# Kernel optimization log

Hardware: AMD Instinct MI355X
Metric: run time of the kernel (lower is better)

Reference implementation:

```python
import jax, jax.numpy as jnp
import numpy as np

B, N, C, H = 8, 128, 256, 8
HS = C // H
SCALE = HS ** -0.5
EPS = 1e-5


def layernorm(x, w, b):
    mu = jnp.mean(x, axis=-1, keepdims=True)
    var = jnp.var(x, axis=-1, keepdims=True)
    return (x - mu) * jax.lax.rsqrt(var + EPS) * w + b


def setup_inputs() -> dict:
    key = jax.random.key(0)
    ks = jax.random.split(key, 12)
    inp = {
        "joint_feature": jax.random.normal(ks[0], (B, N, C), jnp.float32),
        "relation_feature": jax.random.normal(ks[1], (B, N, N, C), jnp.float32),
        "conn_feature": jax.random.uniform(ks[2], (B, N, N), jnp.float32),
        # LayerNorm params
        "ln1_w": jnp.ones((C,), jnp.float32), "ln1_b": jnp.zeros((C,), jnp.float32),
        "ln2_w": jnp.ones((C,), jnp.float32), "ln2_b": jnp.zeros((C,), jnp.float32),
        "ln3_w": jnp.ones((C,), jnp.float32), "ln3_b": jnp.zeros((C,), jnp.float32),
        # Attention params (qkv_bias=False)
        "qkv_w": 0.02 * jax.random.normal(ks[3], (3 * C, C), jnp.float32),
        "rconv_w": 0.02 * jax.random.normal(ks[4], (H, C), jnp.float32),
        "proj_w": 0.02 * jax.random.normal(ks[5], (C, C), jnp.float32),
        "proj_b": jnp.zeros((C,), jnp.float32),
        # Mlp params (hidden_features == dim in this Block)
        "fc1_w": 0.02 * jax.random.normal(ks[6], (C, C), jnp.float32),
        "fc1_b": jnp.zeros((C,), jnp.float32),
        "fc2_w": 0.02 * jax.random.normal(ks[7], (C, C), jnp.float32),
        "fc2_b": jnp.zeros((C,), jnp.float32),
    }
    return inp


def reference(joint_feature, relation_feature, conn_feature,
              ln1_w, ln1_b, ln2_w, ln2_b, ln3_w, ln3_b,
              qkv_w, rconv_w, proj_w, proj_b,
              fc1_w, fc1_b, fc2_w, fc2_b):
    # --- Attention branch ---
    jn = layernorm(joint_feature, ln1_w, ln1_b)          # [B,N,C]
    rn = layernorm(relation_feature, ln2_w, ln2_b)       # [B,N,N,C]
    qkv = jn @ qkv_w.T                                   # [B,N,3C]
    qkv = qkv.reshape(B, N, 3, H, HS)
    q = jnp.transpose(qkv[:, :, 0], (0, 2, 1, 3))        # [B,H,N,HS]
    k = jnp.transpose(qkv[:, :, 1], (0, 2, 1, 3))
    v = jnp.transpose(qkv[:, :, 2], (0, 2, 1, 3))
    attn_J = jnp.einsum('bhnd,bhmd->bhnm', q, k)         # [B,H,N,N]
    attn_R = jnp.einsum('bnmc,hc->bhnm', rn, rconv_w)    # [B,H,N,N]
    attn = (attn_J + attn_R) * conn_feature[:, None] * SCALE
    attn = jax.nn.softmax(attn, axis=-1)
    x = jnp.einsum('bhnm,bhmd->bnhd', attn, v).reshape(B, N, C)
    x = x @ proj_w.T + proj_b
    joint = joint_feature + x
    # --- MLP branch (hidden = dim, exact GELU as torch nn.GELU) ---
    h = layernorm(joint, ln3_w, ln3_b)
    h = jax.nn.gelu(h @ fc1_w.T + fc1_b, approximate=False)
    h = h @ fc2_w.T + fc2_b
    return joint + h
```

## Files before the change

kernel.cpp:

```cpp
#include <hip/hip_runtime.h>
#include <hip/hip_bf16.h>

#define Bb 8
#define Nn 128
#define Cc 256
#define SCALE 0.1767766952966369f
#define EPS 1e-5f

typedef short v8s __attribute__((ext_vector_type(8)));
typedef short v4s __attribute__((ext_vector_type(4)));
typedef float v4f __attribute__((ext_vector_type(4)));
using bf16_t = __hip_bfloat16;

__device__ inline float bf2f(bf16_t h){ return __bfloat162float(h); }
__device__ inline short f2bfbits(float f){
    unsigned int u = __float_as_uint(f);
    u += 0x7fff + ((u >> 16) & 1u);
    return (short)(u >> 16);
}

__device__ inline float rscatter8(const float (&S)[8], int l){
    bool b0 = l & 1, b1 = l & 2, b2 = l & 4;
    float t[4];
#pragma unroll
    for (int k = 0; k < 4; k++){
        float keep = b0 ? S[k+4] : S[k];
        float give = b0 ? S[k]   : S[k+4];
        t[k] = keep + __shfl_xor(give, 1);
    }
    float u[2];
#pragma unroll
    for (int k = 0; k < 2; k++){
        float keep = b1 ? t[k+2] : t[k];
        float give = b1 ? t[k]   : t[k+2];
        u[k] = keep + __shfl_xor(give, 2);
    }
    float r;
    {
        float keep = b2 ? u[1] : u[0];
        float give = b2 ? u[0] : u[1];
        r = keep + __shfl_xor(give, 4);
    }
    r += __shfl_xor(r, 8);
    r += __shfl_xor(r, 16);
    return r;
}

template<int NTOT, int EPI>
__device__ __forceinline__ void lngemm_body(
        const float* __restrict__ A, const float* __restrict__ lnw,
        const float* __restrict__ lnb, const float* __restrict__ W,
        const float* __restrict__ bias, short* __restrict__ out,
        int mtile, int ntile0)
{
    __shared__ short a_s[16][264];
    __shared__ float red[2][16][16];
    const int t = threadIdx.x;
    const int r = t >> 4, j = t & 15;
    const float* rowp = A + (size_t)(mtile + r) * Cc + j * 16;
    float x[16];
#pragma unroll
    for (int i = 0; i < 4; i++){
        float4 v = *(const float4*)(rowp + i * 4);
        x[i*4+0]=v.x; x[i*4+1]=v.y; x[i*4+2]=v.z; x[i*4+3]=v.w;
    }
    float s1 = 0.f, s2 = 0.f;
#pragma unroll
    for (int i = 0; i < 16; i++){ s1 += x[i]; s2 = fmaf(x[i], x[i], s2); }
    red[0][r][j] = s1; red[1][r][j] = s2;
    __syncthreads();
    float t1 = 0.f, t2 = 0.f;
#pragma unroll
    for (int i = 0; i < 16; i++){ t1 += red[0][r][i]; t2 += red[1][r][i]; }
    const float mu = t1 * (1.f/256.f);
    const float rstd = rsqrtf(t2 * (1.f/256.f) - mu*mu + EPS);
    short pk[16];
#pragma unroll
    for (int i = 0; i < 4; i++){
        float4 wv4 = *(const float4*)(lnw + j*16 + i*4);
        float4 bv4 = *(const float4*)(lnb + j*16 + i*4);
        pk[i*4+0] = f2bfbits((x[i*4+0]-mu)*rstd*wv4.x + bv4.x);
        pk[i*4+1] = f2bfbits((x[i*4+1]-mu)*rstd*wv4.y + bv4.y);
        pk[i*4+2] = f2bfbits((x[i*4+2]-mu)*rstd*wv4.z + bv4.z);
        pk[i*4+3] = f2bfbits((x[i*4+3]-mu)*rstd*wv4.w + bv4.w);
    }
    *(v8s*)&a_s[r][j*16]     = *(v8s*)&pk[0];
    *(v8s*)&a_s[r][j*16 + 8] = *(v8s*)&pk[8];
    __syncthreads();

    const int lane = t & 63;
    const int wv = t >> 6;
    const int ntile = ntile0 + wv * 16;
    const int mi = lane & 15, q = lane >> 4;
    const short* alds = &a_s[mi][q * 8];
    const float* wp = W + (size_t)(ntile + mi) * Cc + q * 8;
    v4f acc = {0.f, 0.f, 0.f, 0.f};
#pragma unroll
    for (int kk = 0; kk < 8; kk++){
        v8s af = *(const v8s*)(alds + kk * 32);
        float4 w0 = *(const float4*)(wp + kk * 32);
        float4 w1 = *(const float4*)(wp + kk * 32 + 4);
        v8s bf;
        bf[0]=f2bfbits(w0.x); bf[1]=f2bfbits(w0.y); bf[2]=f2bfbits(w0.z); bf[3]=f2bfbits(w0.w);
        bf[4]=f2bfbits(w1.x); bf[5]=f2bfbits(w1.y); bf[6]=f2bfbits(w1.z); bf[7]=f2bfbits(w1.w);
        acc = __builtin_amdgcn_mfma_f32_16x16x32_bf16(af, bf, acc, 0, 0, 0);
    }
    const int n = ntile + mi;
    const float bia = (EPI == 2) ? bias[n] : 0.f;
#pragma unroll
    for (int rr = 0; rr < 4; rr++){
        int m = mtile + q * 4 + rr;
        float v = acc[rr] + bia;
        if (EPI == 2) v = 0.5f * v * (1.f + erff(v * 0.70710678118654752f));
        out[(size_t)m * NTOT + n] = f2bfbits(v);
    }
}

__global__ __launch_bounds__(256) void mega1_kernel(
        const float* __restrict__ rel,
        const float* __restrict__ ln2w, const float* __restrict__ ln2b,
        const float* __restrict__ rconv, short* __restrict__ R,
        const float* __restrict__ joint,
        const float* __restrict__ ln1w, const float* __restrict__ ln1b,
        const float* __restrict__ qkvw, short* __restrict__ qkvb)
{
    if (blockIdx.x >= 2048){
        const int bx = blockIdx.x - 2048;
        lngemm_body<768, 0>(joint, ln1w, ln1b, qkvw, nullptr, qkvb,
                            (bx & 63) * 16, (bx >> 6) * 64);
        return;
    }
    const int lane = threadIdx.x & 63;
    const int hl = lane & 31;
    const int c0 = hl * 8;

    float w2[8][8];
    float Tp[8] = {0,0,0,0,0,0,0,0};
    float Bp[8] = {0,0,0,0,0,0,0,0};
#pragma unroll
    for (int j = 0; j < 8; j++){
        float lw = ln2w[c0 + j];
        float lb = ln2b[c0 + j];
#pragma unroll
        for (int hh = 0; hh < 8; hh++){
            float rc = rconv[hh * Cc + c0 + j];
            w2[j][hh] = lw * rc;
            Tp[hh] += w2[j][hh];
            Bp[hh] = fmaf(lb, rc, Bp[hh]);
        }
    }
    const float Th = rscatter8(Tp, hl);
    const float Bh = rscatter8(Bp, hl);
    const int h = (hl & 1) * 4 + ((hl >> 1) & 1) * 2 + ((hl >> 2) & 1);

    const int hw = (blockIdx.x * 256 + threadIdx.x) >> 5;
    const int hwStride = (2048 * 256) >> 5;
    const int totalRows = Bb * Nn * Nn;

    for (int row = hw; row < totalRows; row += hwStride){
        const float* rp = rel + (size_t)row * Cc + c0;
        float4 xa = *(const float4*)(rp);
        float4 xb = *(const float4*)(rp + 4);
        float x[8] = { xa.x, xa.y, xa.z, xa.w, xb.x, xb.y, xb.z, xb.w };
        float sum = 0.f, sq = 0.f;
        float S[8] = {0,0,0,0,0,0,0,0};
#pragma unroll
        for (int j = 0; j < 8; j++){
            float xv = x[j];
            sum += xv;
            sq = fmaf(xv, xv, sq);
#pragma unroll
            for (int hh = 0; hh < 8; hh++)
                S[hh] = fmaf(xv, w2[j][hh], S[hh]);
        }
#pragma unroll
        for (int o = 1; o <= 16; o <<= 1){
            sum += __shfl_xor(sum, o);
            sq  += __shfl_xor(sq,  o);
        }
        float mu = sum * (1.f / 256.f);
        float rstd = rsqrtf(sq * (1.f / 256.f) - mu * mu + EPS);
        float Sh = rscatter8(S, hl);
        if (hl < 8)
            R[(size_t)row * 8 + h] = f2bfbits(rstd * (Sh - mu * Th) + Bh);
    }
}

template<int EPI>
__global__ __launch_bounds__(256) void gemm_kernel(
        const bf16_t* __restrict__ A, const float* __restrict__ W,
        const float* __restrict__ bias, const float* __restrict__ res,
        float* __restrict__ out)
{
    const int lane = threadIdx.x & 63;
    const int wv = threadIdx.x >> 6;
    const int mtile = blockIdx.x * 16;
    const int ntile = blockIdx.y * 64 + wv * 16;
    const int mi = lane & 15, q = lane >> 4;
    const bf16_t* ap = A + (size_t)(mtile + mi) * Cc + q * 8;
    const float* wp = W + (size_t)(ntile + mi) * Cc + q * 8;
    v4f acc = {0.f, 0.f, 0.f, 0.f};
#pragma unroll
    for (int kk = 0; kk < 8; kk++){
        v8s af = *(const v8s*)(ap + kk * 32);
        float4 w0 = *(const float4*)(wp + kk * 32);
        float4 w1 = *(const float4*)(wp + kk * 32 + 4);
        v8s bf;
        bf[0]=f2bfbits(w0.x); bf[1]=f2bfbits(w0.y); bf[2]=f2bfbits(w0.z); bf[3]=f2bfbits(w0.w);
        bf[4]=f2bfbits(w1.x); bf[5]=f2bfbits(w1.y); bf[6]=f2bfbits(w1.z); bf[7]=f2bfbits(w1.w);
        acc = __builtin_amdgcn_mfma_f32_16x16x32_bf16(af, bf, acc, 0, 0, 0);
    }
    const int n = ntile + mi;
    const float bia = bias[n];
#pragma unroll
    for (int r = 0; r < 4; r++){
        int m = mtile + q * 4 + r;
        float v = acc[r] + bia + res[(size_t)m * Cc + n];
        out[(size_t)m * Cc + n] = v;
    }
}

__global__ __launch_bounds__(256) void fc1_kernel(
        const float* __restrict__ joint2,
        const float* __restrict__ ln3w, const float* __restrict__ ln3b,
        const float* __restrict__ fc1w, const float* __restrict__ fc1b,
        short* __restrict__ h2)
{
    lngemm_body<256, 2>(joint2, ln3w, ln3b, fc1w, fc1b, h2,
                        blockIdx.x * 16, blockIdx.y * 64);
}

__global__ __launch_bounds__(256) void attn_kernel(
        const bf16_t* __restrict__ qkv,
        const bf16_t* __restrict__ R,
        const float* __restrict__ conn,
        short* __restrict__ xatt)
{
    const int bid = blockIdx.x;
    const int b = bid >> 5;
    const int h = (bid >> 2) & 7;
    const int nq = bid & 3;
    __shared__ float k_s[128 * 36];
    __shared__ float v_s[128 * 32];
    __shared__ float q_s[32 * 33];
    __shared__ float p_s[32 * 132];
    const int t = threadIdx.x;
    const bf16_t* qkvb = qkv + (size_t)b * Nn * 768;

#pragma unroll
    for (int i = 0; i < 16; i++){
        int idx = t + i * 256;
        int m = idx >> 5, d = idx & 31;
        k_s[m * 36 + d] = bf2f(qkvb[m * 768 + 256 + h * 32 + d]);
        v_s[m * 32 + d] = bf2f(qkvb[m * 768 + 512 + h * 32 + d]);
    }
#pragma unroll
    for (int i = 0; i < 4; i++){
        int idx = t + i * 256;
        int nl = idx >> 5, d = idx & 31;
        q_s[nl * 33 + d] = bf2f(qkvb[(nq * 32 + nl) * 768 + h * 32 + d]);
    }
    __syncthreads();

    const int nl = t >> 3, tg = t & 7;
    const int n = nq * 32 + nl;
    float qr[32];
#pragma unroll
    for (int d = 0; d < 32; d++) qr[d] = q_s[nl * 33 + d];
    const bf16_t* Rrow = R + ((size_t)(b * Nn + n) * Nn) * 8 + h;
    const float* crow = conn + (size_t)(b * Nn + n) * Nn;

    float s[16];
#pragma unroll
    for (int i = 0; i < 16; i++){
        int m = tg + 8 * i;
        float acc = 0.f;
#pragma unroll
        for (int g = 0; g < 8; g++){
            float4 kv = *(const float4*)&k_s[m * 36 + g * 4];
            acc = fmaf(qr[g*4+0], kv.x, acc);
            acc = fmaf(qr[g*4+1], kv.y, acc);
            acc = fmaf(qr[g*4+2], kv.z, acc);
            acc = fmaf(qr[g*4+3], kv.w, acc);
        }
        s[i] = (acc + bf2f(Rrow[(size_t)m * 8])) * crow[m] * SCALE;
    }
    float mx = s[0];
#pragma unroll
    for (int i = 1; i < 16; i++) mx = fmaxf(mx, s[i]);
    mx = fmaxf(mx, __shfl_xor(mx, 1));
    mx = fmaxf(mx, __shfl_xor(mx, 2));
    mx = fmaxf(mx, __shfl_xor(mx, 4));
    float lsum = 0.f;
#pragma unroll
    for (int i = 0; i < 16; i++){ s[i] = expf(s[i] - mx); lsum += s[i]; }
    lsum += __shfl_xor(lsum, 1);
    lsum += __shfl_xor(lsum, 2);
    lsum += __shfl_xor(lsum, 4);
    float inv = 1.f / lsum;
#pragma unroll
    for (int i = 0; i < 16; i++)
        p_s[nl * 132 + tg + 8 * i] = s[i] * inv;
    __syncthreads();

    const int d0 = tg * 4;
    float a0 = 0.f, a1 = 0.f, a2 = 0.f, a3 = 0.f;
    for (int m = 0; m < 128; m++){
        float p = p_s[nl * 132 + m];
        float4 vv = *(const float4*)&v_s[m * 32 + d0];
        a0 = fmaf(p, vv.x, a0);
        a1 = fmaf(p, vv.y, a1);
        a2 = fmaf(p, vv.z, a2);
        a3 = fmaf(p, vv.w, a3);
    }
    v4s o4; o4[0]=f2bfbits(a0); o4[1]=f2bfbits(a1); o4[2]=f2bfbits(a2); o4[3]=f2bfbits(a3);
    *(v4s*)(xatt + (size_t)(b * Nn + n) * Cc + h * 32 + d0) = o4;
}

extern "C" void kernel_launch(void* const* d_in, const int* in_sizes, int n_in,
                              void* d_out, int out_size, void* d_ws, size_t ws_size,
                              hipStream_t stream)
{
    const float* joint  = (const float*)d_in[0];
    const float* rel    = (const float*)d_in[1];
    const float* conn   = (const float*)d_in[2];
    const float* ln1w   = (const float*)d_in[3];
    const float* ln1b   = (const float*)d_in[4];
    const float* ln2w   = (const float*)d_in[5];
    const float* ln2b   = (const float*)d_in[6];
    const float* ln3w   = (const float*)d_in[7];
    const float* ln3b   = (const float*)d_in[8];
    const float* qkvw   = (const float*)d_in[9];
    const float* rconv  = (const float*)d_in[10];
    const float* projw  = (const float*)d_in[11];
    const float* projb  = (const float*)d_in[12];
    const float* fc1w   = (const float*)d_in[13];
    const float* fc1b   = (const float*)d_in[14];
    const float* fc2w   = (const float*)d_in[15];
    const float* fc2b   = (const float*)d_in[16];

    char* w = (char*)d_ws;
    short* Rb     = (short*)(w);
    short* qkvb   = (short*)(w + 2097152);
    short* xattb  = (short*)(w + 3670016);
    float* joint2 = (float*)(w + 4194304);
    short* h2b    = (short*)(w + 5242880);

    mega1_kernel<<<dim3(2816), dim3(256), 0, stream>>>(
        rel, ln2w, ln2b, rconv, Rb, joint, ln1w, ln1b, qkvw, qkvb);
    attn_kernel<<<dim3(256), dim3(256), 0, stream>>>(
        (const bf16_t*)qkvb, (const bf16_t*)Rb, conn, xattb);
    gemm_kernel<1><<<dim3(64, 4), dim3(256), 0, stream>>>(
        (const bf16_t*)xattb, projw, projb, joint, joint2);
    fc1_kernel<<<dim3(64, 4), dim3(256), 0, stream>>>(
        joint2, ln3w, ln3b, fc1w, fc1b, h2b);
    gemm_kernel<3><<<dim3(64, 4), dim3(256), 0, stream>>>(
        (const bf16_t*)h2b, fc2w, fc2b, joint2, (float*)d_out);
}
```

Before: 258.7 us.

## Fuse proj, LN3, fc1+GELU and fc2 into one tail kernel per row tile

Replaces three separate launches (proj GEMM with residual, LN3+fc1+GELU, fc2 GEMM with residual) with a single tail kernel. Each block owns 16 rows and all 256 output columns, keeping joint2 and the hidden activations in shared memory instead of round-tripping through global workspace. This removes two launches and the intermediate global traffic. In exchange, the grid shrinks from 256 to 64 blocks, which lowers parallelism, and each block now reads the full weight matrices.

```diff
diff --git a/kernel.cpp b/kernel.cpp
--- a/kernel.cpp
+++ b/kernel.cpp
@@ -46,12 +46,11 @@
     return r;
 }
 
-template<int NTOT, int EPI>
+template<int NTOT>
 __device__ __forceinline__ void lngemm_body(
         const float* __restrict__ A, const float* __restrict__ lnw,
         const float* __restrict__ lnb, const float* __restrict__ W,
-        const float* __restrict__ bias, short* __restrict__ out,
-        int mtile, int ntile0)
+        short* __restrict__ out, int mtile, int ntile0)
 {
     __shared__ short a_s[16][264];
     __shared__ float red[2][16][16];
@@ -106,13 +105,10 @@
         acc = __builtin_amdgcn_mfma_f32_16x16x32_bf16(af, bf, acc, 0, 0, 0);
     }
     const int n = ntile + mi;
-    const float bia = (EPI == 2) ? bias[n] : 0.f;
 #pragma unroll
     for (int rr = 0; rr < 4; rr++){
         int m = mtile + q * 4 + rr;
-        float v = acc[rr] + bia;
-        if (EPI == 2) v = 0.5f * v * (1.f + erff(v * 0.70710678118654752f));
-        out[(size_t)m * NTOT + n] = f2bfbits(v);
+        out[(size_t)m * NTOT + n] = f2bfbits(acc[rr]);
     }
 }
 
@@ -126,8 +122,8 @@
 {
     if (blockIdx.x >= 2048){
         const int bx = blockIdx.x - 2048;
-        lngemm_body<768, 0>(joint, ln1w, ln1b, qkvw, nullptr, qkvb,
-                            (bx & 63) * 16, (bx >> 6) * 64);
+        lngemm_body<768>(joint, ln1w, ln1b, qkvw, qkvb,
+                         (bx & 63) * 16, (bx >> 6) * 64);
         return;
     }
     const int lane = threadIdx.x & 63;
@@ -184,50 +180,6 @@
         if (hl < 8)
             R[(size_t)row * 8 + h] = f2bfbits(rstd * (Sh - mu * Th) + Bh);
     }
-}
-
-template<int EPI>
-__global__ __launch_bounds__(256) void gemm_kernel(
-        const bf16_t* __restrict__ A, const float* __restrict__ W,
-        const float* __restrict__ bias, const float* __restrict__ res,
-        float* __restrict__ out)
-{
-    const int lane = threadIdx.x & 63;
-    const int wv = threadIdx.x >> 6;
-    const int mtile = blockIdx.x * 16;
-    const int ntile = blockIdx.y * 64 + wv * 16;
-    const int mi = lane & 15, q = lane >> 4;
-    const bf16_t* ap = A + (size_t)(mtile + mi) * Cc + q * 8;
-    const float* wp = W + (size_t)(ntile + mi) * Cc + q * 8;
-    v4f acc = {0.f, 0.f, 0.f, 0.f};
-#pragma unroll
-    for (int kk = 0; kk < 8; kk++){
-        v8s af = *(const v8s*)(ap + kk * 32);
-        float4 w0 = *(const float4*)(wp + kk * 32);
-        float4 w1 = *(const float4*)(wp + kk * 32 + 4);
-        v8s bf;
-        bf[0]=f2bfbits(w0.x); bf[1]=f2bfbits(w0.y); bf[2]=f2bfbits(w0.z); bf[3]=f2bfbits(w0.w);
-        bf[4]=f2bfbits(w1.x); bf[5]=f2bfbits(w1.y); bf[6]=f2bfbits(w1.z); bf[7]=f2bfbits(w1.w);
-        acc = __builtin_amdgcn_mfma_f32_16x16x32_bf16(af, bf, acc, 0, 0, 0);
-    }
-    const int n = ntile + mi;
-    const float bia = bias[n];
-#pragma unroll
-    for (int r = 0; r < 4; r++){
-        int m = mtile + q * 4 + r;
-        float v = acc[r] + bia + res[(size_t)m * Cc + n];
-        out[(size_t)m * Cc + n] = v;
-    }
-}
-
-__global__ __launch_bounds__(256) void fc1_kernel(
-        const float* __restrict__ joint2,
-        const float* __restrict__ ln3w, const float* __restrict__ ln3b,
-        const float* __restrict__ fc1w, const float* __restrict__ fc1b,
-        short* __restrict__ h2)
-{
-    lngemm_body<256, 2>(joint2, ln3w, ln3b, fc1w, fc1b, h2,
-                        blockIdx.x * 16, blockIdx.y * 64);
 }
 
 __global__ __launch_bounds__(256) void attn_kernel(
@@ -315,6 +267,148 @@
     }
     v4s o4; o4[0]=f2bfbits(a0); o4[1]=f2bfbits(a1); o4[2]=f2bfbits(a2); o4[3]=f2bfbits(a3);
     *(v4s*)(xatt + (size_t)(b * Nn + n) * Cc + h * 32 + d0) = o4;
+}
+
+__global__ __launch_bounds__(256) void tail_kernel(
+        const bf16_t* __restrict__ xatt,
+        const float* __restrict__ projw, const float* __restrict__ projb,
+        const float* __restrict__ joint,
+        const float* __restrict__ ln3w, const float* __restrict__ ln3b,
+        const float* __restrict__ fc1w, const float* __restrict__ fc1b,
+        const float* __restrict__ fc2w, const float* __restrict__ fc2b,
+        float* __restrict__ out)
+{
+    __shared__ float j2_s[16][260];
+    __shared__ short a_s[16][264];
+    __shared__ float red[2][16][16];
+    const int t = threadIdx.x;
+    const int mtile = blockIdx.x * 16;
+    const int lane = t & 63;
+    const int wv = t >> 6;
+    const int mi = lane & 15, q = lane >> 4;
+    const int nbase = wv * 64;
+
+    {
+        const bf16_t* ap = xatt + (size_t)(mtile + mi) * Cc + q * 8;
+        v4f acc[4] = {{0,0,0,0},{0,0,0,0},{0,0,0,0},{0,0,0,0}};
+#pragma unroll
+        for (int kk = 0; kk < 8; kk++){
+            v8s af = *(const v8s*)(ap + kk * 32);
+#pragma unroll
+            for (int sub = 0; sub < 4; sub++){
+                const float* wp = projw + (size_t)(nbase + sub * 16 + mi) * Cc + q * 8 + kk * 32;
+                float4 w0 = *(const float4*)(wp);
+                float4 w1 = *(const float4*)(wp + 4);
+                v8s bf;
+                bf[0]=f2bfbits(w0.x); bf[1]=f2bfbits(w0.y); bf[2]=f2bfbits(w0.z); bf[3]=f2bfbits(w0.w);
+                bf[4]=f2bfbits(w1.x); bf[5]=f2bfbits(w1.y); bf[6]=f2bfbits(w1.z); bf[7]=f2bfbits(w1.w);
+                acc[sub] = __builtin_amdgcn_mfma_f32_16x16x32_bf16(af, bf, acc[sub], 0, 0, 0);
+            }
+        }
+#pragma unroll
+        for (int sub = 0; sub < 4; sub++){
+            const int n = nbase + sub * 16 + mi;
+            const float bia = projb[n];
+#pragma unroll
+            for (int rr = 0; rr < 4; rr++){
+                int m = q * 4 + rr;
+                j2_s[m][n] = acc[sub][rr] + bia + joint[(size_t)(mtile + m) * Cc + n];
+            }
+        }
+    }
+    __syncthreads();
+
+    {
+        const int r = t >> 4, j = t & 15;
+        float x[16];
+#pragma unroll
+        for (int i = 0; i < 16; i++) x[i] = j2_s[r][j * 16 + i];
+        float s1 = 0.f, s2 = 0.f;
+#pragma unroll
+        for (int i = 0; i < 16; i++){ s1 += x[i]; s2 = fmaf(x[i], x[i], s2); }
+        red[0][r][j] = s1; red[1][r][j] = s2;
+        __syncthreads();
+        float t1 = 0.f, t2 = 0.f;
+#pragma unroll
+        for (int i = 0; i < 16; i++){ t1 += red[0][r][i]; t2 += red[1][r][i]; }
+        const float mu = t1 * (1.f/256.f);
+        const float rstd = rsqrtf(t2 * (1.f/256.f) - mu*mu + EPS);
+        short pk[16];
+#pragma unroll
+        for (int i = 0; i < 4; i++){
+            float4 wv4 = *(const float4*)(ln3w + j*16 + i*4);
+            float4 bv4 = *(const float4*)(ln3b + j*16 + i*4);
+            pk[i*4+0] = f2bfbits((x[i*4+0]-mu)*rstd*wv4.x + bv4.x);
+            pk[i*4+1] = f2bfbits((x[i*4+1]-mu)*rstd*wv4.y + bv4.y);
+            pk[i*4+2] = f2bfbits((x[i*4+2]-mu)*rstd*wv4.z + bv4.z);
+            pk[i*4+3] = f2bfbits((x[i*4+3]-mu)*rstd*wv4.w + bv4.w);
+        }
+        *(v8s*)&a_s[r][j*16]     = *(v8s*)&pk[0];
+        *(v8s*)&a_s[r][j*16 + 8] = *(v8s*)&pk[8];
+    }
+    __syncthreads();
+
+    {
+        const short* alds = &a_s[mi][q * 8];
+        v4f acc[4] = {{0,0,0,0},{0,0,0,0},{0,0,0,0},{0,0,0,0}};
+#pragma unroll
+        for (int kk = 0; kk < 8; kk++){
+            v8s af = *(const v8s*)(alds + kk * 32);
+#pragma unroll
+            for (int sub = 0; sub < 4; sub++){
+                const float* wp = fc1w + (size_t)(nbase + sub * 16 + mi) * Cc + q * 8 + kk * 32;
+                float4 w0 = *(const float4*)(wp);
+                float4 w1 = *(const float4*)(wp + 4);
+                v8s bf;
+                bf[0]=f2bfbits(w0.x); bf[1]=f2bfbits(w0.y); bf[2]=f2bfbits(w0.z); bf[3]=f2bfbits(w0.w);
+                bf[4]=f2bfbits(w1.x); bf[5]=f2bfbits(w1.y); bf[6]=f2bfbits(w1.z); bf[7]=f2bfbits(w1.w);
+                acc[sub] = __builtin_amdgcn_mfma_f32_16x16x32_bf16(af, bf, acc[sub], 0, 0, 0);
+            }
+        }
+        __syncthreads();
+#pragma unroll
+        for (int sub = 0; sub < 4; sub++){
+            const int n = nbase + sub * 16 + mi;
+            const float bia = fc1b[n];
+#pragma unroll
+            for (int rr = 0; rr < 4; rr++){
+                int m = q * 4 + rr;
+                float v = acc[sub][rr] + bia;
+                v = 0.5f * v * (1.f + erff(v * 0.70710678118654752f));
+                a_s[m][n] = f2bfbits(v);
+            }
+        }
+    }
+    __syncthreads();
+
+    {
+        const short* alds = &a_s[mi][q * 8];
+        v4f acc[4] = {{0,0,0,0},{0,0,0,0},{0,0,0,0},{0,0,0,0}};
+#pragma unroll
+        for (int kk = 0; kk < 8; kk++){
+            v8s af = *(const v8s*)(alds + kk * 32);
+#pragma unroll
+            for (int sub = 0; sub < 4; sub++){
+                const float* wp = fc2w + (size_t)(nbase + sub * 16 + mi) * Cc + q * 8 + kk * 32;
+                float4 w0 = *(const float4*)(wp);
+                float4 w1 = *(const float4*)(wp + 4);
+                v8s bf;
+                bf[0]=f2bfbits(w0.x); bf[1]=f2bfbits(w0.y); bf[2]=f2bfbits(w0.z); bf[3]=f2bfbits(w0.w);
+                bf[4]=f2bfbits(w1.x); bf[5]=f2bfbits(w1.y); bf[6]=f2bfbits(w1.z); bf[7]=f2bfbits(w1.w);
+                acc[sub] = __builtin_amdgcn_mfma_f32_16x16x32_bf16(af, bf, acc[sub], 0, 0, 0);
+            }
+        }
+#pragma unroll
+        for (int sub = 0; sub < 4; sub++){
+            const int n = nbase + sub * 16 + mi;
+            const float bia = fc2b[n];
+#pragma unroll
+            for (int rr = 0; rr < 4; rr++){
+                int m = q * 4 + rr;
+                out[(size_t)(mtile + m) * Cc + n] = acc[sub][rr] + bia + j2_s[m][n];
+            }
+        }
+    }
 }
 
 extern "C" void kernel_launch(void* const* d_in, const int* in_sizes, int n_in,
@@ -343,17 +437,12 @@
     short* Rb     = (short*)(w);
     short* qkvb   = (short*)(w + 2097152);
     short* xattb  = (short*)(w + 3670016);
-    float* joint2 = (float*)(w + 4194304);
-    short* h2b    = (short*)(w + 5242880);
 
     mega1_kernel<<<dim3(2816), dim3(256), 0, stream>>>(
         rel, ln2w, ln2b, rconv, Rb, joint, ln1w, ln1b, qkvw, qkvb);
     attn_kernel<<<dim3(256), dim3(256), 0, stream>>>(
         (const bf16_t*)qkvb, (const bf16_t*)Rb, conn, xattb);
-    gemm_kernel<1><<<dim3(64, 4), dim3(256), 0, stream>>>(
-        (const bf16_t*)xattb, projw, projb, joint, joint2);
-    fc1_kernel<<<dim3(64, 4), dim3(256), 0, stream>>>(
-        joint2, ln3w, ln3b, fc1w, fc1b, h2b);
-    gemm_kernel<3><<<dim3(64, 4), dim3(256), 0, stream>>>(
-        (const bf16_t*)h2b, fc2w, fc2b, joint2, (float*)d_out);
-}
+    tail_kernel<<<dim3(64), dim3(256), 0, stream>>>(
+        (const bf16_t*)xattb, projw, projb, joint, ln3w, ln3b,
+        fc1w, fc1b, fc2w, fc2b, (float*)d_out);
+}
```

After: 268.8 us. +3.9%, slower.
